# Kernel optimization log

Measured on AMD Instinct MI355X. Metric: run time of the kernel, lower is better.

## Reference

```python
import jax, jax.numpy as jnp
import numpy as np

N_NODES = 100000


def gcn_conv(x, src, dst, W, b, n_nodes):
    """PyG GCNConv: out = D^{-1/2} (A + I) D^{-1/2} (x @ W) + b.
    src/dst are the original (non-self-loop) edges; self loops handled analytically.
    """
    h = x @ W  # [N, out]
    ones = jnp.ones(src.shape[0], dtype=h.dtype)
    # degree including self loop
    deg = jax.ops.segment_sum(ones, dst, num_segments=n_nodes) + 1.0  # [N]
    dinv = jax.lax.rsqrt(deg)
    norm = dinv[src] * dinv[dst]  # [E]
    msg = h[src] * norm[:, None]  # gather + scale
    agg = jax.ops.segment_sum(msg, dst, num_segments=n_nodes)  # scatter-add
    # self-loop contribution: norm = deg^{-1/2} * deg^{-1/2} = 1/deg
    agg = agg + h * (1.0 / deg)[:, None]
    return agg + b


def setup_inputs() -> dict:
    key = jax.random.key(0)
    k1, k2, k3, k4 = jax.random.split(key, 4)
    n, e = N_NODES, 3200000
    x = jax.random.normal(k1, (n, 256), dtype=jnp.float32)
    edge_index = jax.random.randint(k2, (2, e), 0, n, dtype=jnp.int64)
    W1 = jax.random.normal(k3, (256, 64), dtype=jnp.float32) * (1.0 / np.sqrt(256))
    b1 = jnp.zeros((64,), dtype=jnp.float32)
    W2 = jax.random.normal(k4, (64, 4), dtype=jnp.float32) * (1.0 / np.sqrt(64))
    b2 = jnp.zeros((4,), dtype=jnp.float32)
    return {"x": x, "edge_index": edge_index, "W1": W1, "b1": b1, "W2": W2, "b2": b2}


def reference(x, edge_index, W1, b1, W2, b2):
    n = x.shape[0]
    src, dst = edge_index[0], edge_index[1]
    h = gcn_conv(x, src, dst, W1, b1, n)
    h = jax.nn.leaky_relu(h, negative_slope=0.01)  # nn.LeakyReLU default
    # F.dropout in eval mode is identity
    h = gcn_conv(h, src, dst, W2, b2, n)
    return jax.nn.softmax(h, axis=1)
```

## Files before the change

### kernel.cpp

```cpp
#include <hip/hip_runtime.h>
#include <hip/hip_bf16.h>
#include <math.h>


#define NB 256
#define MAXB 512
#define SCHUNK 12544

typedef __attribute__((ext_vector_type(8))) short bf16x8;
typedef __attribute__((ext_vector_type(4))) float f32x4;
typedef __attribute__((ext_vector_type(2))) float f32x2;

__device__ __forceinline__ int edge_val(const void* ep, size_t idx, int is64) {
    if (is64) return (int)(((const long long*)ep)[idx]);
    return ((const int*)ep)[idx];
}

__device__ __forceinline__ unsigned short f2bf(float f) {
    unsigned int u = __float_as_uint(f);
    return (unsigned short)((u + 0x7FFFu + ((u >> 16) & 1u)) >> 16);
}

__device__ __forceinline__ void acc_fp8row(unsigned int r, float& a0, float& a1,
                                           float& a2, float& a3) {
    const f32x2 lo = __builtin_amdgcn_cvt_pk_f32_fp8((int)r, false);
    const f32x2 hi = __builtin_amdgcn_cvt_pk_f32_fp8((int)r, true);
    a0 += lo[0]; a1 += lo[1]; a2 += hi[0]; a3 += hi[1];
}

__device__ __forceinline__ unsigned char f32_to_fp8(float f) {
    const int enc = __builtin_amdgcn_cvt_pk_fp8_f32(f, 0.f, 0, false);
    return (unsigned char)(enc & 0xff);
}

__global__ void detect_width(const unsigned int* __restrict__ ew, int* __restrict__ flag) {
    const int i = threadIdx.x;
    const unsigned long long m = __ballot(ew[2 * i + 1] != 0u);
    if (i == 0) *flag = (m == 0ull) ? 1 : 0;
}

__global__ __launch_bounds__(256) void hist_pass(
    const void* __restrict__ edges, int E, const int* __restrict__ flagp,
    int* __restrict__ ghist, int B) {
    __shared__ int hist[MAXB];
    const int tid = threadIdx.x;
    for (int i = tid; i < B; i += 256) hist[i] = 0;
    __syncthreads();
    const int is64 = *flagp;
    const int per = (E + NB - 1) / NB;
    const int s0 = blockIdx.x * per;
    const int s1 = min(s0 + per, E);
    for (int i = s0 + tid; i < s1; i += 256) {
        const int d = edge_val(edges, (size_t)E + i, is64);
        atomicAdd(&hist[d >> 8], 1);
    }
    __syncthreads();
    for (int i = tid; i < B; i += 256) ghist[(size_t)blockIdx.x * B + i] = hist[i];
}

__global__ __launch_bounds__(NB) void col_scan(
    const int* __restrict__ ghist, int* __restrict__ goff,
    int* __restrict__ bsum, int B) {
    __shared__ int sm[NB];
    const int tid = threadIdx.x;
    const int b = blockIdx.x;
    const int v = ghist[(size_t)tid * B + b];
    sm[tid] = v;
    __syncthreads();
    for (int off = 1; off < NB; off <<= 1) {
        int val = (tid >= off) ? sm[tid - off] : 0;
        __syncthreads();
        sm[tid] += val;
        __syncthreads();
    }
    goff[(size_t)tid * B + b] = sm[tid] - v;
    if (tid == NB - 1) bsum[b] = sm[tid];
}

__global__ __launch_bounds__(512) void base_scan(
    const int* __restrict__ bsum, int* __restrict__ bbase,
    int* __restrict__ row_ptr, int B, int n, int E) {
    __shared__ int sm[512];
    const int tid = threadIdx.x;
    const int v = (tid < B) ? bsum[tid] : 0;
    sm[tid] = v;
    __syncthreads();
    for (int off = 1; off < 512; off <<= 1) {
        int val = (tid >= off) ? sm[tid - off] : 0;
        __syncthreads();
        sm[tid] += val;
        __syncthreads();
    }
    if (tid < B) bbase[tid] = sm[tid] - v;
    if (tid == 0) { bbase[B] = E; row_ptr[n] = E; }
}

__global__ __launch_bounds__(512) void scatter_pass(
    const void* __restrict__ edges, int E, const int* __restrict__ flagp,
    const int* __restrict__ ghist, const int* __restrict__ goff,
    const int* __restrict__ bbase, unsigned int* __restrict__ ebuf, int B) {
    __shared__ unsigned int buf[SCHUNK];
    __shared__ int lb[MAXB];
    __shared__ int lf[MAXB];
    __shared__ int sm[MAXB];
    const int tid = threadIdx.x;
    const int blk = blockIdx.x;
    const int is64 = *flagp;
    const int per = (E + NB - 1) / NB;
    const int s0 = blk * per;
    const int s1 = min(s0 + per, E);

    if (per <= SCHUNK) {
        const int c = (tid < B) ? ghist[(size_t)blk * B + tid] : 0;
        sm[tid] = c;
        __syncthreads();
        for (int off = 1; off < MAXB; off <<= 1) {
            int val = (tid >= off) ? sm[tid - off] : 0;
            __syncthreads();
            sm[tid] += val;
            __syncthreads();
        }
        if (tid < B) { lb[tid] = sm[tid] - c; lf[tid] = sm[tid] - c; }
        __syncthreads();
        for (int i = s0 + tid; i < s1; i += 512) {
            const int d = edge_val(edges, (size_t)E + i, is64);
            const int s = edge_val(edges, (size_t)i, is64);
            const unsigned int val = ((unsigned int)s << 8) | (unsigned int)(d & 255);
            const int pos = atomicAdd(&lf[d >> 8], 1);
            buf[pos] = val;
        }
        __syncthreads();
        const int lane = tid & 63;
        const int wv = tid >> 6;
        for (int b = wv; b < B; b += 8) {
            const int lo = lb[b];
            const int cnt = lf[b] - lo;
            if (cnt > 0) {
                unsigned int* dst = ebuf + bbase[b] + goff[(size_t)blk * B + b];
                for (int k = lane; k < cnt; k += 64) dst[k] = buf[lo + k];
            }
        }
    } else {
        for (int i = tid; i < B; i += 512)
            lf[i] = bbase[i] + goff[(size_t)blk * B + i];
        __syncthreads();
        for (int i = s0 + tid; i < s1; i += 512) {
            const int d = edge_val(edges, (size_t)E + i, is64);
            const int s = edge_val(edges, (size_t)i, is64);
            const int pos = atomicAdd(&lf[d >> 8], 1);
            ebuf[pos] = ((unsigned int)s << 8) | (unsigned int)(d & 255);
        }
    }
}

__global__ __launch_bounds__(512) void bucket_csr(
    const unsigned int* __restrict__ ebuf, const int* __restrict__ bbase,
    int* __restrict__ row_ptr, float* __restrict__ dinv,
    int* __restrict__ col_src, int n) {
    __shared__ int hist[256];
    __shared__ int scn[256];
    __shared__ int fill[256];
    const int tid = threadIdx.x;
    const int b = blockIdx.x;
    if (tid < 256) hist[tid] = 0;
    __syncthreads();
    const int base = bbase[b];
    const int m = bbase[b + 1] - base;
    const unsigned int* eb = ebuf + base;
    for (int i = tid; i < m; i += 512) atomicAdd(&hist[eb[i] & 255u], 1);
    __syncthreads();
    if (tid < 256) scn[tid] = hist[tid];
    __syncthreads();
    for (int off = 1; off < 256; off <<= 1) {
        int val = 0;
        if (tid < 256 && tid >= off) val = scn[tid - off];
        __syncthreads();
        if (tid < 256) scn[tid] += val;
        __syncthreads();
    }
    if (tid < 256) {
        const int excl = scn[tid] - hist[tid];
        fill[tid] = excl;
        const int v = b * 256 + tid;
        if (v < n) {
            row_ptr[v] = base + excl;
            dinv[v] = rsqrtf((float)hist[tid] + 1.0f);
        }
    }
    __syncthreads();
    for (int i = tid; i < m; i += 512) {
        const unsigned int e = eb[i];
        const int p = atomicAdd(&fill[e & 255u], 1);
        col_src[base + p] = (int)(e >> 8);
    }
}

__global__ __launch_bounds__(256) void gemm1_kernel(
    const float* __restrict__ x, const float* __restrict__ W1,
    const float* __restrict__ dinv, unsigned char* __restrict__ hs1f8, int n) {
    __shared__ unsigned short wt[64 * 264];
    const int tid = threadIdx.x;
    for (int i = tid; i < 4096; i += 256) {
        const int k = i >> 4;
        const int c0 = (i & 15) * 4;
        const float4 w = *((const float4*)W1 + i);
        wt[(c0 + 0) * 264 + k] = f2bf(w.x);
        wt[(c0 + 1) * 264 + k] = f2bf(w.y);
        wt[(c0 + 2) * 264 + k] = f2bf(w.z);
        wt[(c0 + 3) * 264 + k] = f2bf(w.w);
    }
    __syncthreads();

    const int lane = tid & 63;
    const int wid = tid >> 6;
    const int row0 = blockIdx.x * 64 + wid * 16;
    const int rr = lane & 15;
    const int kh = lane >> 4;

    union FragU { bf16x8 v; unsigned short u[8]; };
    bf16x8 af[8];
    {
        int r = row0 + rr;
        if (r >= n) r = n - 1;
        const float* xr = x + (size_t)r * 256 + kh * 8;
#pragma unroll
        for (int ks = 0; ks < 8; ++ks) {
            const float4 p0 = *(const float4*)(xr + ks * 32);
            const float4 p1 = *(const float4*)(xr + ks * 32 + 4);
            FragU f;
            f.u[0] = f2bf(p0.x); f.u[1] = f2bf(p0.y);
            f.u[2] = f2bf(p0.z); f.u[3] = f2bf(p0.w);
            f.u[4] = f2bf(p1.x); f.u[5] = f2bf(p1.y);
            f.u[6] = f2bf(p1.z); f.u[7] = f2bf(p1.w);
            af[ks] = f.v;
        }
    }
    f32x4 acc[4];
#pragma unroll
    for (int ct = 0; ct < 4; ++ct) acc[ct] = (f32x4){0.f, 0.f, 0.f, 0.f};
#pragma unroll
    for (int ct = 0; ct < 4; ++ct) {
        const unsigned short* wcol = wt + (ct * 16 + rr) * 264 + kh * 8;
#pragma unroll
        for (int ks = 0; ks < 8; ++ks) {
            const bf16x8 bf = *(const bf16x8*)(wcol + ks * 32);
            acc[ct] = __builtin_amdgcn_mfma_f32_16x16x32_bf16(af[ks], bf, acc[ct], 0, 0, 0);
        }
    }
#pragma unroll
    for (int j = 0; j < 4; ++j) {
        const int gr = row0 + kh * 4 + j;
        if (gr < n) {
            const float dv = dinv[gr];
#pragma unroll
            for (int ct = 0; ct < 4; ++ct)
                hs1f8[(size_t)gr * 64 + ct * 16 + rr] = f32_to_fp8(acc[ct][j] * dv);
        }
    }
}

__global__ __launch_bounds__(256) void agg1_kernel(
    const int* __restrict__ row_ptr, const int* __restrict__ col_src,
    const unsigned char* __restrict__ hs1f8, const float* __restrict__ dinv,
    const float* __restrict__ b1, const float* __restrict__ W2,
    float* __restrict__ hs2, int n) {
    const int tid = threadIdx.x;
    const int q = tid & 15;
    const int v = blockIdx.x * 16 + (tid >> 4);
    if (v >= n) return;
    const int rs = row_ptr[v];
    const int re = row_ptr[v + 1];
    float a0 = 0.f, a1 = 0.f, a2 = 0.f, a3 = 0.f;
    int e = rs;
    for (; e + 16 <= re; e += 16) {
        const int cs = col_src[e + q];
        unsigned int r[16];
#pragma unroll
        for (int j = 0; j < 16; ++j) {
            const int s = __shfl(cs, j, 16);
            r[j] = *(const unsigned int*)(hs1f8 + (size_t)s * 64 + q * 4);
        }
#pragma unroll
        for (int j = 0; j < 16; ++j) acc_fp8row(r[j], a0, a1, a2, a3);
    }
    const int rem = re - e;
    if (rem > 0) {
        const int cs = col_src[(q < rem) ? e + q : re - 1];
        for (int j = 0; j < rem; ++j) {
            const int s = __shfl(cs, j, 16);
            const unsigned int r = *(const unsigned int*)(hs1f8 + (size_t)s * 64 + q * 4);
            acc_fp8row(r, a0, a1, a2, a3);
        }
    }
    float s0 = 0.f, s1 = 0.f, s2 = 0.f, s3 = 0.f;
    acc_fp8row(*(const unsigned int*)(hs1f8 + (size_t)v * 64 + q * 4), s0, s1, s2, s3);
    const float dv = dinv[v];
    const float4 bb = ((const float4*)b1)[q];
    float4 res;
    res.x = dv * (a0 + s0) + bb.x;
    res.y = dv * (a1 + s1) + bb.y;
    res.z = dv * (a2 + s2) + bb.z;
    res.w = dv * (a3 + s3) + bb.w;
    res.x = res.x > 0.f ? res.x : 0.01f * res.x;
    res.y = res.y > 0.f ? res.y : 0.01f * res.y;
    res.z = res.z > 0.f ? res.z : 0.01f * res.z;
    res.w = res.w > 0.f ? res.w : 0.01f * res.w;
    const float4* W2v = (const float4*)W2;
    const float4 w0 = W2v[q * 4 + 0], w1 = W2v[q * 4 + 1];
    const float4 w2 = W2v[q * 4 + 2], w3 = W2v[q * 4 + 3];
    float4 p;
    p.x = res.x * w0.x + res.y * w1.x + res.z * w2.x + res.w * w3.x;
    p.y = res.x * w0.y + res.y * w1.y + res.z * w2.y + res.w * w3.y;
    p.z = res.x * w0.z + res.y * w1.z + res.z * w2.z + res.w * w3.z;
    p.w = res.x * w0.w + res.y * w1.w + res.z * w2.w + res.w * w3.w;
#pragma unroll
    for (int s = 1; s < 16; s <<= 1) {
        p.x += __shfl_xor(p.x, s, 16); p.y += __shfl_xor(p.y, s, 16);
        p.z += __shfl_xor(p.z, s, 16); p.w += __shfl_xor(p.w, s, 16);
    }
    if (q == 0) {
        float4 o; o.x = p.x * dv; o.y = p.y * dv; o.z = p.z * dv; o.w = p.w * dv;
        *(float4*)(hs2 + (size_t)v * 4) = o;
    }
}

__global__ __launch_bounds__(256) void agg2_kernel(
    const int* __restrict__ row_ptr, const int* __restrict__ col_src,
    const float* __restrict__ hs2, const float* __restrict__ dinv,
    const float* __restrict__ b2, float* __restrict__ out, int n) {
    const int lane = threadIdx.x & 63;
    int v = blockIdx.x * 4 + (threadIdx.x >> 6);
    v = __builtin_amdgcn_readfirstlane(v);
    if (v >= n) return;
    const int c = lane & 3;
    const int ei = lane >> 2;
    const int rs = row_ptr[v];
    const int re = row_ptr[v + 1];
    float acc = 0.f;
    for (int e0 = rs; e0 < re; e0 += 16) {
        const int e = e0 + ei;
        if (e < re) {
            const int s = col_src[e];
            acc += hs2[(size_t)s * 4 + c];
        }
    }
    acc += __shfl_xor(acc, 4);
    acc += __shfl_xor(acc, 8);
    acc += __shfl_xor(acc, 16);
    acc += __shfl_xor(acc, 32);
    const float val = dinv[v] * (acc + hs2[(size_t)v * 4 + c]) + b2[c];
    float m = fmaxf(val, __shfl_xor(val, 1));
    m = fmaxf(m, __shfl_xor(m, 2));
    const float ex = __expf(val - m);
    float s = ex + __shfl_xor(ex, 1);
    s += __shfl_xor(s, 2);
    if (lane < 4) out[(size_t)v * 4 + c] = ex / s;
}

extern "C" void kernel_launch(void* const* d_in, const int* in_sizes, int n_in,
                              void* d_out, int out_size, void* d_ws, size_t ws_size,
                              hipStream_t stream) {
    const float* x  = (const float*)d_in[0];
    const void*  ei = d_in[1];
    const float* W1 = (const float*)d_in[2];
    const float* b1 = (const float*)d_in[3];
    const float* W2 = (const float*)d_in[4];
    const float* b2 = (const float*)d_in[5];
    const int n = in_sizes[0] / 256;
    const int E = in_sizes[1] / 2;
    const int B = (n + 255) / 256;

    char* ws = (char*)d_ws;
    size_t off = 0;
    auto alloc = [&](size_t bytes) -> void* {
        void* p = ws + off;
        off += (bytes + 255) & ~(size_t)255;
        return p;
    };
    int*   flag    = (int*)alloc(sizeof(int) * 64);
    int*   ghist   = (int*)alloc(sizeof(int) * (size_t)NB * B);
    int*   goff    = (int*)alloc(sizeof(int) * (size_t)NB * B);
    int*   bsum    = (int*)alloc(sizeof(int) * B);
    int*   bbase   = (int*)alloc(sizeof(int) * (B + 1));
    int*   row_ptr = (int*)alloc(sizeof(int) * (n + 1));
    int*   col_src = (int*)alloc(sizeof(int) * (size_t)E);
    float* dinv    = (float*)alloc(sizeof(float) * n);
    unsigned char* hs1f8 = (unsigned char*)alloc(sizeof(unsigned char) * (size_t)n * 64);
    float* hs2     = (float*)alloc(sizeof(float) * (size_t)n * 4);
    unsigned int* ebuf = (unsigned int*)alloc(sizeof(unsigned int) * (size_t)E);
    (void)n_in; (void)out_size; (void)ws_size;

    detect_width<<<1, 64, 0, stream>>>((const unsigned int*)ei, flag);
    hist_pass<<<NB, 256, 0, stream>>>(ei, E, flag, ghist, B);
    col_scan<<<B, NB, 0, stream>>>(ghist, goff, bsum, B);
    base_scan<<<1, 512, 0, stream>>>(bsum, bbase, row_ptr, B, n, E);
    scatter_pass<<<NB, 512, 0, stream>>>(ei, E, flag, ghist, goff, bbase, ebuf, B);
    bucket_csr<<<B, 512, 0, stream>>>(ebuf, bbase, row_ptr, dinv, col_src, n);
    gemm1_kernel<<<(n + 63) / 64, 256, 0, stream>>>(x, W1, dinv, hs1f8, n);
    agg1_kernel<<<(n + 15) / 16, 256, 0, stream>>>(row_ptr, col_src, hs1f8, dinv, b1, W2, hs2, n);
    agg2_kernel<<<(n + 3) / 4, 256, 0, stream>>>(row_ptr, col_src, hs2, dinv, b2, (float*)d_out, n);
}
```

Baseline: 188.2 us.

## Split CSR rows by source half and add nontemporal streaming loads

The bucket CSR build now sorts each row's edges into two groups by whether the source index falls in the lower or upper half of the node range, and records a per-node midpoint. agg1 walks the two groups separately in 8-edge batches, so gathers from hs1f8 are clustered by source region for better cache locality. Streaming reads of x and col_src now use nontemporal loads so they do not evict gathered feature data. The cost is a 512-bin scan in bucket_csr, an extra midpoint array, and smaller gather batches with more tail handling per node.

```diff
diff --git a/kernel.cpp b/kernel.cpp
--- a/kernel.cpp
+++ b/kernel.cpp
@@ -10,6 +10,7 @@
 typedef __attribute__((ext_vector_type(8))) short bf16x8;
 typedef __attribute__((ext_vector_type(4))) float f32x4;
 typedef __attribute__((ext_vector_type(2))) float f32x2;
+typedef __attribute__((ext_vector_type(4))) float nf4;
 
 __device__ __forceinline__ int edge_val(const void* ep, size_t idx, int is64) {
     if (is64) return (int)(((const long long*)ep)[idx]);
@@ -155,42 +156,47 @@
 
 __global__ __launch_bounds__(512) void bucket_csr(
     const unsigned int* __restrict__ ebuf, const int* __restrict__ bbase,
-    int* __restrict__ row_ptr, float* __restrict__ dinv,
-    int* __restrict__ col_src, int n) {
-    __shared__ int hist[256];
-    __shared__ int scn[256];
-    __shared__ int fill[256];
+    int* __restrict__ row_ptr, int* __restrict__ midp, float* __restrict__ dinv,
+    int* __restrict__ col_src, int n, int half) {
+    __shared__ int hist[512];
+    __shared__ int scn[512];
+    __shared__ int fill[512];
     const int tid = threadIdx.x;
     const int b = blockIdx.x;
-    if (tid < 256) hist[tid] = 0;
+    hist[tid] = 0;
     __syncthreads();
     const int base = bbase[b];
     const int m = bbase[b + 1] - base;
     const unsigned int* eb = ebuf + base;
-    for (int i = tid; i < m; i += 512) atomicAdd(&hist[eb[i] & 255u], 1);
-    __syncthreads();
-    if (tid < 256) scn[tid] = hist[tid];
-    __syncthreads();
-    for (int off = 1; off < 256; off <<= 1) {
-        int val = 0;
-        if (tid < 256 && tid >= off) val = scn[tid - off];
-        __syncthreads();
-        if (tid < 256) scn[tid] += val;
-        __syncthreads();
-    }
+    for (int i = tid; i < m; i += 512) {
+        const unsigned int e = eb[i];
+        const int key = (int)((e & 255u) << 1) | ((int)(e >> 8) >= half ? 1 : 0);
+        atomicAdd(&hist[key], 1);
+    }
+    __syncthreads();
+    scn[tid] = hist[tid];
+    __syncthreads();
+    for (int off = 1; off < 512; off <<= 1) {
+        int val = (tid >= off) ? scn[tid - off] : 0;
+        __syncthreads();
+        scn[tid] += val;
+        __syncthreads();
+    }
+    fill[tid] = scn[tid] - hist[tid];
+    __syncthreads();
     if (tid < 256) {
-        const int excl = scn[tid] - hist[tid];
-        fill[tid] = excl;
         const int v = b * 256 + tid;
         if (v < n) {
-            row_ptr[v] = base + excl;
-            dinv[v] = rsqrtf((float)hist[tid] + 1.0f);
+            row_ptr[v] = base + fill[2 * tid];
+            midp[v]    = base + fill[2 * tid + 1];
+            dinv[v] = rsqrtf((float)(hist[2 * tid] + hist[2 * tid + 1]) + 1.0f);
         }
     }
     __syncthreads();
     for (int i = tid; i < m; i += 512) {
         const unsigned int e = eb[i];
-        const int p = atomicAdd(&fill[e & 255u], 1);
+        const int key = (int)((e & 255u) << 1) | ((int)(e >> 8) >= half ? 1 : 0);
+        const int p = atomicAdd(&fill[key], 1);
         col_src[base + p] = (int)(e >> 8);
     }
 }
@@ -225,13 +231,13 @@
         const float* xr = x + (size_t)r * 256 + kh * 8;
 #pragma unroll
         for (int ks = 0; ks < 8; ++ks) {
-            const float4 p0 = *(const float4*)(xr + ks * 32);
-            const float4 p1 = *(const float4*)(xr + ks * 32 + 4);
+            const nf4 p0 = __builtin_nontemporal_load((const nf4*)(xr + ks * 32));
+            const nf4 p1 = __builtin_nontemporal_load((const nf4*)(xr + ks * 32 + 4));
             FragU f;
-            f.u[0] = f2bf(p0.x); f.u[1] = f2bf(p0.y);
-            f.u[2] = f2bf(p0.z); f.u[3] = f2bf(p0.w);
-            f.u[4] = f2bf(p1.x); f.u[5] = f2bf(p1.y);
-            f.u[6] = f2bf(p1.z); f.u[7] = f2bf(p1.w);
+            f.u[0] = f2bf(p0[0]); f.u[1] = f2bf(p0[1]);
+            f.u[2] = f2bf(p0[2]); f.u[3] = f2bf(p0[3]);
+            f.u[4] = f2bf(p1[0]); f.u[5] = f2bf(p1[1]);
+            f.u[6] = f2bf(p1[2]); f.u[7] = f2bf(p1[3]);
             af[ks] = f.v;
         }
     }
@@ -260,7 +266,8 @@
 }
 
 __global__ __launch_bounds__(256) void agg1_kernel(
-    const int* __restrict__ row_ptr, const int* __restrict__ col_src,
+    const int* __restrict__ row_ptr, const int* __restrict__ midp,
+    const int* __restrict__ col_src,
     const unsigned char* __restrict__ hs1f8, const float* __restrict__ dinv,
     const float* __restrict__ b1, const float* __restrict__ W2,
     float* __restrict__ hs2, int n) {
@@ -269,29 +276,43 @@
     const int v = blockIdx.x * 16 + (tid >> 4);
     if (v >= n) return;
     const int rs = row_ptr[v];
+    const int md = midp[v];
     const int re = row_ptr[v + 1];
     float a0 = 0.f, a1 = 0.f, a2 = 0.f, a3 = 0.f;
-    int e = rs;
-    for (; e + 16 <= re; e += 16) {
-        const int cs = col_src[e + q];
-        unsigned int r[16];
-#pragma unroll
-        for (int j = 0; j < 16; ++j) {
-            const int s = __shfl(cs, j, 16);
-            r[j] = *(const unsigned int*)(hs1f8 + (size_t)s * 64 + q * 4);
-        }
-#pragma unroll
-        for (int j = 0; j < 16; ++j) acc_fp8row(r[j], a0, a1, a2, a3);
-    }
-    const int rem = re - e;
-    if (rem > 0) {
-        const int cs = col_src[(q < rem) ? e + q : re - 1];
-        for (int j = 0; j < rem; ++j) {
-            const int s = __shfl(cs, j, 16);
-            const unsigned int r = *(const unsigned int*)(hs1f8 + (size_t)s * 64 + q * 4);
-            acc_fp8row(r, a0, a1, a2, a3);
-        }
-    }
+
+    auto run = [&](int s, int t) {
+        int e = s;
+        for (; e + 8 <= t; e += 8) {
+            const int cs = __builtin_nontemporal_load(col_src + e + (q & 7));
+            unsigned int r[8];
+#pragma unroll
+            for (int j = 0; j < 8; ++j) {
+                const int sj = __shfl(cs, j, 16);
+                r[j] = *(const unsigned int*)(hs1f8 + (size_t)sj * 64 + q * 4);
+            }
+#pragma unroll
+            for (int j = 0; j < 8; ++j) acc_fp8row(r[j], a0, a1, a2, a3);
+        }
+        const int rem = t - e;
+        if (rem > 0) {
+            const int cs = __builtin_nontemporal_load(
+                col_src + ((q < rem) ? e + q : t - 1));
+            unsigned int r[8];
+#pragma unroll
+            for (int j = 0; j < 8; ++j) {
+                if (j < rem) {
+                    const int sj = __shfl(cs, j, 16);
+                    r[j] = *(const unsigned int*)(hs1f8 + (size_t)sj * 64 + q * 4);
+                }
+            }
+#pragma unroll
+            for (int j = 0; j < 8; ++j)
+                if (j < rem) acc_fp8row(r[j], a0, a1, a2, a3);
+        }
+    };
+    run(rs, md);
+    run(md, re);
+
     float s0 = 0.f, s1 = 0.f, s2 = 0.f, s3 = 0.f;
     acc_fp8row(*(const unsigned int*)(hs1f8 + (size_t)v * 64 + q * 4), s0, s1, s2, s3);
     const float dv = dinv[v];
@@ -340,7 +361,7 @@
     for (int e0 = rs; e0 < re; e0 += 16) {
         const int e = e0 + ei;
         if (e < re) {
-            const int s = col_src[e];
+            const int s = __builtin_nontemporal_load(col_src + e);
             acc += hs2[(size_t)s * 4 + c];
         }
     }
@@ -369,6 +390,7 @@
     const int n = in_sizes[0] / 256;
     const int E = in_sizes[1] / 2;
     const int B = (n + 255) / 256;
+    const int half = n >> 1;
 
     char* ws = (char*)d_ws;
     size_t off = 0;
@@ -383,6 +405,7 @@
     int*   bsum    = (int*)alloc(sizeof(int) * B);
     int*   bbase   = (int*)alloc(sizeof(int) * (B + 1));
     int*   row_ptr = (int*)alloc(sizeof(int) * (n + 1));
+    int*   midp    = (int*)alloc(sizeof(int) * n);
     int*   col_src = (int*)alloc(sizeof(int) * (size_t)E);
     float* dinv    = (float*)alloc(sizeof(float) * n);
     unsigned char* hs1f8 = (unsigned char*)alloc(sizeof(unsigned char) * (size_t)n * 64);
@@ -395,8 +418,8 @@
     col_scan<<<B, NB, 0, stream>>>(ghist, goff, bsum, B);
     base_scan<<<1, 512, 0, stream>>>(bsum, bbase, row_ptr, B, n, E);
     scatter_pass<<<NB, 512, 0, stream>>>(ei, E, flag, ghist, goff, bbase, ebuf, B);
-    bucket_csr<<<B, 512, 0, stream>>>(ebuf, bbase, row_ptr, dinv, col_src, n);
+    bucket_csr<<<B, 512, 0, stream>>>(ebuf, bbase, row_ptr, midp, dinv, col_src, n, half);
     gemm1_kernel<<<(n + 63) / 64, 256, 0, stream>>>(x, W1, dinv, hs1f8, n);
-    agg1_kernel<<<(n + 15) / 16, 256, 0, stream>>>(row_ptr, col_src, hs1f8, dinv, b1, W2, hs2, n);
+    agg1_kernel<<<(n + 15) / 16, 256, 0, stream>>>(row_ptr, midp, col_src, hs1f8, dinv, b1, W2, hs2, n);
     agg2_kernel<<<(n + 3) / 4, 256, 0, stream>>>(row_ptr, col_src, hs2, dinv, b2, (float*)d_out, n);
 }
```

New measurement: 201.5 us. +7.1%, slower.
